# Performance work log

Hardware: AMD Instinct MI355X
Metric: run time of the kernel (lower is better)

## Reference

```python
import jax, jax.numpy as jnp
import numpy as np

B, S, H, KVH, D = 1, 2048, 32, 8, 128
ROPE_THETA = 500000.0


def _rotate_half(x):
    x1, x2 = jnp.split(x, 2, axis=-1)
    return jnp.concatenate((-x2, x1), axis=-1)


def setup_inputs() -> dict:
    key = jax.random.key(0)
    ks = jax.random.split(key, 5)
    hidden_states = jax.random.normal(ks[0], (B, S, H * D), dtype=jnp.float32)
    Wq = jax.random.normal(ks[1], (H * D, H * D), dtype=jnp.float32) * 0.02
    Wk = jax.random.normal(ks[2], (KVH * D, H * D), dtype=jnp.float32) * 0.02
    Wv = jax.random.normal(ks[3], (KVH * D, H * D), dtype=jnp.float32) * 0.02
    Wo = jax.random.normal(ks[4], (H * D, H * D), dtype=jnp.float32) * 0.02
    # rotary tables (Llama-style, concat of freqs with itself)
    inv_freq = 1.0 / (ROPE_THETA ** (jnp.arange(0, D, 2, dtype=jnp.float32) / D))
    freqs = jnp.arange(S, dtype=jnp.float32)[:, None] * inv_freq[None, :]  # [S, D/2]
    emb = jnp.concatenate((freqs, freqs), axis=-1)  # [S, D]
    cos = jnp.cos(emb)[None]  # [1, S, D]
    sin = jnp.sin(emb)[None]
    # additive causal mask, matching SDPA attn_mask semantics
    causal = jnp.tril(jnp.ones((S, S), dtype=bool))
    attention_mask = jnp.where(causal, 0.0, -1e9).astype(jnp.float32)[None, None]  # [1,1,S,S]
    return {"hidden_states": hidden_states, "attention_mask": attention_mask,
            "cos": cos, "sin": sin, "Wq": Wq, "Wk": Wk, "Wv": Wv, "Wo": Wo}


def reference(hidden_states, attention_mask, cos, sin, Wq, Wk, Wv, Wo):
    b, s, _ = hidden_states.shape
    d = cos.shape[-1]
    h = Wq.shape[0] // d
    kvh = Wk.shape[0] // d
    g = h // kvh  # GQA group size

    # fused QKV projection (nn.Linear: y = x @ W^T), then split heads -> [b, heads, s, d]
    q = jnp.einsum('bsi,oi->bso', hidden_states, Wq).reshape(b, s, h, d).transpose(0, 2, 1, 3)
    k = jnp.einsum('bsi,oi->bso', hidden_states, Wk).reshape(b, s, kvh, d).transpose(0, 2, 1, 3)
    v = jnp.einsum('bsi,oi->bso', hidden_states, Wv).reshape(b, s, kvh, d).transpose(0, 2, 1, 3)

    # rotary embedding (unsqueeze_dim=1)
    c = cos[:, None]  # [b,1,s,d]
    sn = sin[:, None]
    q = q * c + _rotate_half(q) * sn
    k = k * c + _rotate_half(k) * sn

    # GQA: view q as [b, kvh, g, s, d]; contract against un-repeated k/v
    qg = q.reshape(b, kvh, g, s, d)
    scale = 1.0 / jnp.sqrt(jnp.float32(d))
    scores = jnp.einsum('bkgsd,bktd->bkgst', qg, k) * scale  # [b,kvh,g,s,s]
    scores = scores + attention_mask[:, :, None]  # broadcast [b,1,1,s,s]
    probs = jax.nn.softmax(scores, axis=-1)
    attn = jnp.einsum('bkgst,bktd->bkgsd', probs, v)  # [b,kvh,g,s,d]

    attn = attn.reshape(b, h, s, d).transpose(0, 2, 1, 3).reshape(b, s, h * d)
    out = jnp.einsum('bso,po->bsp', attn, Wo)
    return out
```

## Files before the change

kernel.cpp:

```cpp
#include <hip/hip_runtime.h>
#include <hip/hip_bf16.h>

#define SEQ 2048
#define HD  128
#define NH  32
#define NKV 8
#define MODEL 4096
#define KVDIM 1024
#define QKVN 6144

typedef __attribute__((ext_vector_type(8))) short short8;
typedef __attribute__((ext_vector_type(4))) short short4v;
typedef __attribute__((ext_vector_type(4))) float float4v;

#define MFMA16(a, b, c) __builtin_amdgcn_mfma_f32_16x16x32_bf16(a, b, c, 0, 0, 0)

__device__ __forceinline__ short f2bf(float x) {
  unsigned u = __builtin_bit_cast(unsigned, x);
  u += 0x7fffu + ((u >> 16) & 1u);
  return (short)(u >> 16);
}
__device__ __forceinline__ float bf2f(short s) {
  unsigned u = ((unsigned)(unsigned short)s) << 16;
  return __builtin_bit_cast(float, u);
}

__device__ __forceinline__ void async_copy16(const void* g, void* l) {
  __builtin_amdgcn_global_load_lds((const __attribute__((address_space(1))) void*)g,
                                   (__attribute__((address_space(3))) void*)l, 16, 0, 0);
}

__global__ __launch_bounds__(256) void cast_bf16(const float* __restrict__ in,
                                                 short* __restrict__ out, int n) {
  int i = (blockIdx.x * 256 + threadIdx.x) * 4;
  if (i < n) {
    float4v v = *(const float4v*)(in + i);
    short4v o;
    o[0] = f2bf(v[0]); o[1] = f2bf(v[1]); o[2] = f2bf(v[2]); o[3] = f2bf(v[3]);
    *(short4v*)(out + i) = o;
  }
}

__global__ __launch_bounds__(512, 2) void gemm256(const short* __restrict__ A,
                                                  const short* __restrict__ B,
                                                  short* __restrict__ C,
                                                  int M, int N, int K) {
  __shared__ __align__(16) short As[2][256 * 64];
  __shared__ __align__(16) short Bs[2][256 * 64];
  const int tid = threadIdx.x;
  const int lane = tid & 63, w = tid >> 6;
  const int col = lane & 15, quad = lane >> 4;
  const int wm = w >> 2, wn = w & 3;

  const int nbx = N >> 8;
  int bid = blockIdx.x, nwg = gridDim.x;
  int swz = (nwg & 7) ? bid : ((bid & 7) * (nwg >> 3) + (bid >> 3));
  const int m0 = (swz / nbx) << 8;
  const int n0 = (swz % nbx) << 8;

  const int srow = tid >> 3;
  const int schunk = (tid & 7) ^ (srow & 7);
  const short* pA = A + (size_t)(m0 + srow) * K + schunk * 8;
  const short* pB = B + (size_t)(n0 + srow) * K + schunk * 8;
  const int ldst = tid * 8;

  const int sw = (col & 7) << 3;
  const int kof0 = (quad * 8) ^ sw;
  const int kof1 = (32 + quad * 8) ^ sw;
  const int ra = wm * 128, rb = wn * 64;

  float4v acc[8][4] = {};
  const int iters = K >> 6;

#define SA(buf, rA, kt) async_copy16(pA + (size_t)(rA) * K + (kt), &As[buf][(rA) * 64 + ldst])
#define SB_(buf, rB, kt) async_copy16(pB + (size_t)(rB) * K + (kt), &Bs[buf][(rB) * 64 + ldst])

  SA(0, 0, 0);  SA(0, 128, 0);
  SB_(0, 0, 0); SB_(0, 64, 0); SB_(0, 128, 0); SB_(0, 192, 0);
  SA(0, 64, 0); SA(0, 192, 0);
  asm volatile("s_waitcnt vmcnt(2)" ::: "memory");
  __builtin_amdgcn_s_barrier();

  for (int t = 0; t < iters; ++t) {
    const int cb = t & 1, nb = cb ^ 1;
    const int kt = (t + 1) << 6;
    const bool pf = (t + 1 < iters);
    const short* a_ = As[cb];
    const short* b_ = Bs[cb];
    short8 af[4][2], bf0[2][2], bf1[2][2];

#pragma unroll
    for (int mi = 0; mi < 4; ++mi) {
      const short* rp = a_ + (ra + mi * 16 + col) * 64;
      af[mi][0] = *(const short8*)(rp + kof0);
      af[mi][1] = *(const short8*)(rp + kof1);
    }
#pragma unroll
    for (int ni = 0; ni < 2; ++ni) {
      const short* rp = b_ + (rb + ni * 16 + col) * 64;
      bf0[ni][0] = *(const short8*)(rp + kof0);
      bf0[ni][1] = *(const short8*)(rp + kof1);
    }
    if (pf) { SA(nb, 0, kt); SA(nb, 128, kt); }
    __builtin_amdgcn_s_barrier();
    asm volatile("s_waitcnt lgkmcnt(0)" ::: "memory");
    __builtin_amdgcn_sched_barrier(0);
    __builtin_amdgcn_s_setprio(1);
#pragma unroll
    for (int mi = 0; mi < 4; ++mi)
#pragma unroll
      for (int ni = 0; ni < 2; ++ni) {
        acc[mi][ni] = MFMA16(af[mi][0], bf0[ni][0], acc[mi][ni]);
        acc[mi][ni] = MFMA16(af[mi][1], bf0[ni][1], acc[mi][ni]);
      }
    __builtin_amdgcn_s_setprio(0);
    __builtin_amdgcn_s_barrier();

#pragma unroll
    for (int ni = 0; ni < 2; ++ni) {
      const short* rp = b_ + (rb + (ni + 2) * 16 + col) * 64;
      bf1[ni][0] = *(const short8*)(rp + kof0);
      bf1[ni][1] = *(const short8*)(rp + kof1);
    }
    if (pf) { SB_(nb, 0, kt); SB_(nb, 64, kt); }
    __builtin_amdgcn_s_barrier();
    asm volatile("s_waitcnt lgkmcnt(0)" ::: "memory");
    __builtin_amdgcn_sched_barrier(0);
    __builtin_amdgcn_s_setprio(1);
#pragma unroll
    for (int mi = 0; mi < 4; ++mi)
#pragma unroll
      for (int ni = 0; ni < 2; ++ni) {
        acc[mi][ni + 2] = MFMA16(af[mi][0], bf1[ni][0], acc[mi][ni + 2]);
        acc[mi][ni + 2] = MFMA16(af[mi][1], bf1[ni][1], acc[mi][ni + 2]);
      }
    __builtin_amdgcn_s_setprio(0);
    if (pf) asm volatile("s_waitcnt vmcnt(4)" ::: "memory");
    else    asm volatile("s_waitcnt vmcnt(0)" ::: "memory");
    __builtin_amdgcn_s_barrier();

#pragma unroll
    for (int mi = 0; mi < 4; ++mi) {
      const short* rp = a_ + (ra + (mi + 4) * 16 + col) * 64;
      af[mi][0] = *(const short8*)(rp + kof0);
      af[mi][1] = *(const short8*)(rp + kof1);
    }
    if (pf) { SB_(nb, 128, kt); SB_(nb, 192, kt); }
    __builtin_amdgcn_s_barrier();
    asm volatile("s_waitcnt lgkmcnt(0)" ::: "memory");
    __builtin_amdgcn_sched_barrier(0);
    __builtin_amdgcn_s_setprio(1);
#pragma unroll
    for (int mi = 0; mi < 4; ++mi)
#pragma unroll
      for (int ni = 0; ni < 2; ++ni) {
        acc[mi + 4][ni + 2] = MFMA16(af[mi][0], bf1[ni][0], acc[mi + 4][ni + 2]);
        acc[mi + 4][ni + 2] = MFMA16(af[mi][1], bf1[ni][1], acc[mi + 4][ni + 2]);
      }
    __builtin_amdgcn_s_setprio(0);
    __builtin_amdgcn_s_barrier();

    if (pf) { SA(nb, 64, kt); SA(nb, 192, kt); }
    __builtin_amdgcn_s_setprio(1);
#pragma unroll
    for (int mi = 0; mi < 4; ++mi)
#pragma unroll
      for (int ni = 0; ni < 2; ++ni) {
        acc[mi + 4][ni] = MFMA16(af[mi][0], bf0[ni][0], acc[mi + 4][ni]);
        acc[mi + 4][ni] = MFMA16(af[mi][1], bf0[ni][1], acc[mi + 4][ni]);
      }
    __builtin_amdgcn_s_setprio(0);
    if (pf) asm volatile("s_waitcnt vmcnt(2)" ::: "memory");
    __builtin_amdgcn_s_barrier();
  }
#undef SA
#undef SB_

#pragma unroll
  for (int mi = 0; mi < 8; ++mi)
#pragma unroll
    for (int ni = 0; ni < 4; ++ni)
#pragma unroll
      for (int r = 0; r < 4; ++r) {
        int row = m0 + ra + mi * 16 + quad * 4 + r;
        int cc  = n0 + rb + ni * 16 + col;
        C[(size_t)row * N + cc] = f2bf(acc[mi][ni][r]);
      }
}

#define BM 128
#define BN 128
#define BK 32

__device__ __forceinline__ void store_out(float* C, size_t idx, float v) { C[idx] = v; }
__device__ __forceinline__ void store_out(short* C, size_t idx, float v) { C[idx] = f2bf(v); }

template <typename OUT>
__global__ __launch_bounds__(256) void gemm_nt(const short* __restrict__ A,
                                               const short* __restrict__ B,
                                               OUT* __restrict__ C,
                                               int M, int N, int K) {
  __shared__ __align__(16) short As[2][BM * BK];
  __shared__ __align__(16) short Bs[2][BN * BK];
  int t = threadIdx.x;
  int w = t >> 6, lane = t & 63;
  int col = lane & 15, quad = lane >> 4;
  int m0 = blockIdx.y * BM, n0 = blockIdx.x * BN;
  int wr = (w >> 1) * 64, wc = (w & 1) * 64;

  int srow   = lane >> 2;
  int schunk = (lane & 3) ^ ((lane >> 3) & 3);
  const short* Ag0 = A + (size_t)(m0 + w * 32 + srow) * K + schunk * 8;
  const short* Ag1 = Ag0 + (size_t)16 * K;
  const short* Bg0 = B + (size_t)(n0 + w * 32 + srow) * K + schunk * 8;
  const short* Bg1 = Bg0 + (size_t)16 * K;
  const int wofs0 = (w * 32) * BK;
  const int wofs1 = (w * 32 + 16) * BK;

  int aswz = (quad ^ ((col >> 1) & 3)) * 8;

  float4v acc[4][4] = {};

  async_copy16(Ag0, &As[0][wofs0]);
  async_copy16(Ag1, &As[0][wofs1]);
  async_copy16(Bg0, &Bs[0][wofs0]);
  async_copy16(Bg1, &Bs[0][wofs1]);
  __syncthreads();

  const int iters = K / BK;
  for (int it = 0; it < iters; it++) {
    const int cb = it & 1, nb = cb ^ 1;
    if (it + 1 < iters) {
      const int k0 = (it + 1) * BK;
      async_copy16(Ag0 + k0, &As[nb][wofs0]);
      async_copy16(Ag1 + k0, &As[nb][wofs1]);
      async_copy16(Bg0 + k0, &Bs[nb][wofs0]);
      async_copy16(Bg1 + k0, &Bs[nb][wofs1]);
    }
    short8 af[4], bfr[4];
#pragma unroll
    for (int i = 0; i < 4; i++)
      af[i] = *(const short8*)&As[cb][(wr + i * 16 + col) * BK + aswz];
#pragma unroll
    for (int i = 0; i < 4; i++)
      bfr[i] = *(const short8*)&Bs[cb][(wc + i * 16 + col) * BK + aswz];
#pragma unroll
    for (int mi = 0; mi < 4; mi++)
#pragma unroll
      for (int ni = 0; ni < 4; ni++)
        acc[mi][ni] = MFMA16(af[mi], bfr[ni], acc[mi][ni]);
    __syncthreads();
  }

#pragma unroll
  for (int mi = 0; mi < 4; mi++)
#pragma unroll
    for (int ni = 0; ni < 4; ni++)
#pragma unroll
      for (int r = 0; r < 4; r++) {
        int row = m0 + wr + mi * 16 + quad * 4 + r;
        int cc  = n0 + wc + ni * 16 + col;
        store_out(C, (size_t)row * N + cc, acc[mi][ni][r]);
      }
}

__global__ __launch_bounds__(128) void rope_kernel(const short* __restrict__ qkv,
                                                   const float* __restrict__ cosp,
                                                   const float* __restrict__ sinp,
                                                   short* __restrict__ qb,
                                                   short* __restrict__ kb) {
  int s = blockIdx.x, head = blockIdx.y, d = threadIdx.x;
  float c  = cosp[s * HD + d];
  float sn = sinp[s * HD + d];
  if (head < NH) {
    const short* base = qkv + (size_t)s * QKVN + head * HD;
    float x = bf2f(base[d]);
    float rot = (d < 64) ? -bf2f(base[d + 64]) : bf2f(base[d - 64]);
    qb[((size_t)(head * SEQ + s)) * HD + d] = f2bf((x * c + rot * sn) * 0.08838834764831845f);
  } else {
    int hk = head - NH;
    const short* base = qkv + (size_t)s * QKVN + MODEL + hk * HD;
    float x = bf2f(base[d]);
    float rot = (d < 64) ? -bf2f(base[d + 64]) : bf2f(base[d - 64]);
    kb[((size_t)(hk * SEQ + s)) * HD + d] = f2bf(x * c + rot * sn);
  }
}

__global__ __launch_bounds__(256) void vtrans_kernel(const short* __restrict__ qkv,
                                                     short* __restrict__ vt) {
  __shared__ short tile[32][34];
  int kv = blockIdx.z;
  int d0 = blockIdx.x * 32, s0 = blockIdx.y * 32;
  int tx = threadIdx.x, ty = threadIdx.y;
#pragma unroll
  for (int j = 0; j < 32; j += 8)
    tile[ty + j][tx] = qkv[(size_t)(s0 + ty + j) * QKVN + MODEL + KVDIM + kv * HD + d0 + tx];
  __syncthreads();
#pragma unroll
  for (int j = 0; j < 32; j += 8)
    vt[((size_t)(kv * HD + d0 + ty + j)) * SEQ + s0 + tx] = tile[tx][ty + j];
}

#define FKT 32
#define KLD 136
#define VLD 40
#define PLD 40

__global__ __launch_bounds__(256, 3) void flash_attn(const short* __restrict__ qb_,
                                                     const short* __restrict__ kb,
                                                     const short* __restrict__ vt,
                                                     short* __restrict__ attn) {
  __shared__ __align__(16) short Ks[2][FKT * KLD];
  __shared__ __align__(16) short Vs[2][HD * VLD];
  __shared__ __align__(16) short Ps[4][32 * PLD];
  const int tid = threadIdx.x;
  const int w = tid >> 6, lane = tid & 63;
  const int col = lane & 15, quad = lane >> 4;
  const int h = blockIdx.x;
  const int kv = h >> 2;
  const int yp = (blockIdx.y < 8) ? (15 - (int)blockIdx.y) : ((int)blockIdx.y - 8);
  const int qB0 = yp * 128;
  const int q0w = qB0 + w * 32;
  const int ntiles = qB0 / FKT + 4;

  short8 ones;
#pragma unroll
  for (int i = 0; i < 8; i++) ones[i] = (short)0x3F80;

  short8 qf[2][4];
  const short* qbase = qb_ + ((size_t)(h * SEQ + q0w + col)) * HD;
#pragma unroll
  for (int rt = 0; rt < 2; rt++)
#pragma unroll
    for (int ks = 0; ks < 4; ks++)
      qf[rt][ks] = *(const short8*)(qbase + rt * 16 * HD + ks * 32 + quad * 8);

  float4v o[2][8] = {};
  float4v la[2] = {};

  const int kg_off = tid * 8;
  const int klds0  = (kg_off >> 7) * KLD + (kg_off & 127);
  const int vd     = tid >> 2;
  const int vkof   = (tid & 3) * 8;
  const size_t vrow0 = ((size_t)(kv * HD + vd)) * SEQ;
  const size_t vrow1 = ((size_t)(kv * HD + vd + 64)) * SEQ;
  const int vlds0 = vd * VLD + vkof;
  const short* kgbase = kb + ((size_t)kv * SEQ) * HD;

  short8 kr0, kr1, vr0, vr1;
  kr0 = *(const short8*)(kgbase + kg_off);
  kr1 = *(const short8*)(kgbase + 2048 + kg_off);
  vr0 = *(const short8*)(vt + vrow0 + vkof);
  vr1 = *(const short8*)(vt + vrow1 + vkof);
  *(short8*)&Ks[0][klds0]            = kr0;
  *(short8*)&Ks[0][klds0 + 16 * KLD] = kr1;
  *(short8*)&Vs[0][vlds0]            = vr0;
  *(short8*)&Vs[0][vlds0 + 64 * VLD] = vr1;
  __syncthreads();

  for (int kt = 0; kt < ntiles; kt++) {
    const int b = kt & 1;
    const int key0 = kt * FKT;
    if (kt + 1 < ntiles) {
      const int nk0 = key0 + FKT;
      const short* kg = kgbase + (size_t)nk0 * HD;
      kr0 = *(const short8*)(kg + kg_off);
      kr1 = *(const short8*)(kg + 2048 + kg_off);
      vr0 = *(const short8*)(vt + vrow0 + nk0 + vkof);
      vr1 = *(const short8*)(vt + vrow1 + nk0 + vkof);
    }
    if (key0 <= q0w + 31) {
      float4v sct[2][2] = {};
#pragma unroll
      for (int ks = 0; ks < 4; ks++) {
        short8 kf0 = *(const short8*)&Ks[b][col * KLD + ks * 32 + quad * 8];
        short8 kf1 = *(const short8*)&Ks[b][(16 + col) * KLD + ks * 32 + quad * 8];
        sct[0][0] = MFMA16(kf0, qf[0][ks], sct[0][0]);
        sct[0][1] = MFMA16(kf0, qf[1][ks], sct[0][1]);
        sct[1][0] = MFMA16(kf1, qf[0][ks], sct[1][0]);
        sct[1][1] = MFMA16(kf1, qf[1][ks], sct[1][1]);
      }
      short* pw = Ps[w];
#pragma unroll
      for (int rt = 0; rt < 2; rt++) {
        int qrow = q0w + rt * 16 + col;
#pragma unroll
        for (int kt2 = 0; kt2 < 2; kt2++) {
          int keyb = key0 + kt2 * 16 + quad * 4;
          short4v p;
#pragma unroll
          for (int r = 0; r < 4; r++) {
            float s = sct[kt2][rt][r];
            if (keyb + r > qrow) s = -INFINITY;
            p[r] = f2bf(__expf(s));
          }
          *(short4v*)&pw[(rt * 16 + col) * PLD + kt2 * 16 + quad * 4] = p;
        }
      }
      asm volatile("s_waitcnt lgkmcnt(0)" ::: "memory");
      short8 pf0 = *(const short8*)&pw[col * PLD + quad * 8];
      short8 pf1 = *(const short8*)&pw[(16 + col) * PLD + quad * 8];
      la[0] = MFMA16(ones, pf0, la[0]);
      la[1] = MFMA16(ones, pf1, la[1]);
#pragma unroll
      for (int nc = 0; nc < 8; nc++) {
        short8 vb = *(const short8*)&Vs[b][(nc * 16 + col) * VLD + quad * 8];
        o[0][nc] = MFMA16(vb, pf0, o[0][nc]);
        o[1][nc] = MFMA16(vb, pf1, o[1][nc]);
      }
    }
    if (kt + 1 < ntiles) {
      const int nb = 1 - b;
      *(short8*)&Ks[nb][klds0]            = kr0;
      *(short8*)&Ks[nb][klds0 + 16 * KLD] = kr1;
      *(short8*)&Vs[nb][vlds0]            = vr0;
      *(short8*)&Vs[nb][vlds0 + 64 * VLD] = vr1;
    }
    __syncthreads();
  }

#pragma unroll
  for (int rt = 0; rt < 2; rt++) {
    float inv = 1.0f / la[rt][0];
    size_t rowbase = (size_t)(q0w + rt * 16 + col) * MODEL + h * HD + quad * 4;
#pragma unroll
    for (int nc = 0; nc < 8; nc++) {
      short4v ov;
#pragma unroll
      for (int r = 0; r < 4; r++) ov[r] = f2bf(o[rt][nc][r] * inv);
      *(short4v*)(attn + rowbase + nc * 16) = ov;
    }
  }
}

extern "C" void kernel_launch(void* const* d_in, const int* in_sizes, int n_in,
                              void* d_out, int out_size, void* d_ws, size_t ws_size,
                              hipStream_t stream) {
  const float* hidden = (const float*)d_in[0];
  const float* cosp = (const float*)d_in[2];
  const float* sinp = (const float*)d_in[3];
  const float* Wq   = (const float*)d_in[4];
  const float* Wk   = (const float*)d_in[5];
  const float* Wv   = (const float*)d_in[6];
  const float* Wo   = (const float*)d_in[7];

  char* ws = (char*)d_ws;
  size_t off = 0;
  auto alloc = [&](size_t bytes) {
    char* p = ws + off;
    off += (bytes + 255) & ~(size_t)255;
    return p;
  };
  short* wq_bf = (short*)alloc((size_t)MODEL * MODEL * 2);
  short* wk_bf = (short*)alloc((size_t)KVDIM * MODEL * 2);
  short* wv_bf = (short*)alloc((size_t)KVDIM * MODEL * 2);
  short* wo_bf = (short*)alloc((size_t)MODEL * MODEL * 2);
  short* h_bf  = (short*)alloc((size_t)SEQ * MODEL * 2);
  short* qkv_bf = (short*)alloc((size_t)SEQ * QKVN * 2);
  short* k_bf  = (short*)alloc((size_t)NKV * SEQ * HD * 2);
  short* v_t   = (short*)alloc((size_t)NKV * HD * SEQ * 2);
  short* attn_bf = (short*)alloc((size_t)SEQ * MODEL * 2);
  short* q_bf    = h_bf;

  {
    int n;
    n = SEQ * MODEL;    cast_bf16<<<n / 1024, 256, 0, stream>>>(hidden, h_bf, n);
    n = MODEL * MODEL;  cast_bf16<<<n / 1024, 256, 0, stream>>>(Wq, wq_bf, n);
    n = KVDIM * MODEL;  cast_bf16<<<n / 1024, 256, 0, stream>>>(Wk, wk_bf, n);
    n = KVDIM * MODEL;  cast_bf16<<<n / 1024, 256, 0, stream>>>(Wv, wv_bf, n);
    n = MODEL * MODEL;  cast_bf16<<<n / 1024, 256, 0, stream>>>(Wo, wo_bf, n);
  }

  gemm256<<<dim3((SEQ / 256) * (QKVN / 256)), 512, 0, stream>>>(h_bf, wq_bf, qkv_bf, SEQ, QKVN, MODEL);

  rope_kernel<<<dim3(SEQ, NH + NKV), 128, 0, stream>>>(qkv_bf, cosp, sinp, q_bf, k_bf);
  vtrans_kernel<<<dim3(HD / 32, SEQ / 32, NKV), dim3(32, 8), 0, stream>>>(qkv_bf, v_t);

  flash_attn<<<dim3(NH, SEQ / 128), 256, 0, stream>>>(q_bf, k_bf, v_t, attn_bf);

  gemm_nt<float><<<dim3(MODEL / BN, SEQ / BM), 256, 0, stream>>>(attn_bf, wo_bf, (float*)d_out, SEQ, MODEL, MODEL);
}
```

Before: 531.2 us.

## Template 256-row GEMM on N-tile width; use it for QKV and output projections

The 256x256 pipelined GEMM becomes a template on the number of 16-wide N fragments per wave. The QKV projection now uses 256x192 tiles, giving 256 workgroups instead of 192, which fills more compute units. The output projection drops the simpler 128x128 double-buffered GEMM and uses the 256x128 pipelined kernel with fp32 stores. The A-fragment loads are now split into four phases of two rows each, which adds barriers, and the smaller B tiles lower arithmetic intensity per workgroup.

```diff
diff --git a/kernel.cpp b/kernel.cpp
--- a/kernel.cpp
+++ b/kernel.cpp
@@ -41,22 +41,27 @@
   }
 }
 
-__global__ __launch_bounds__(512, 2) void gemm256(const short* __restrict__ A,
-                                                  const short* __restrict__ B,
-                                                  short* __restrict__ C,
-                                                  int M, int N, int K) {
+__device__ __forceinline__ void store_out(float* C, size_t idx, float v) { C[idx] = v; }
+__device__ __forceinline__ void store_out(short* C, size_t idx, float v) { C[idx] = f2bf(v); }
+
+template <int NI, typename OUT>
+__global__ __launch_bounds__(512, 2) void gemm256v(const short* __restrict__ A,
+                                                   const short* __restrict__ B,
+                                                   OUT* __restrict__ C,
+                                                   int M, int N, int K) {
+  constexpr int BN = NI * 64;
   __shared__ __align__(16) short As[2][256 * 64];
-  __shared__ __align__(16) short Bs[2][256 * 64];
+  __shared__ __align__(16) short Bs[2][BN * 64];
   const int tid = threadIdx.x;
   const int lane = tid & 63, w = tid >> 6;
   const int col = lane & 15, quad = lane >> 4;
   const int wm = w >> 2, wn = w & 3;
 
-  const int nbx = N >> 8;
+  const int nbx = N / BN;
   int bid = blockIdx.x, nwg = gridDim.x;
   int swz = (nwg & 7) ? bid : ((bid & 7) * (nwg >> 3) + (bid >> 3));
   const int m0 = (swz / nbx) << 8;
-  const int n0 = (swz % nbx) << 8;
+  const int n0 = (swz % nbx) * BN;
 
   const int srow = tid >> 3;
   const int schunk = (tid & 7) ^ (srow & 7);
@@ -67,16 +72,17 @@
   const int sw = (col & 7) << 3;
   const int kof0 = (quad * 8) ^ sw;
   const int kof1 = (32 + quad * 8) ^ sw;
-  const int ra = wm * 128, rb = wn * 64;
-
-  float4v acc[8][4] = {};
+  const int ra = wm * 128, rb = wn * (NI * 16);
+
+  float4v acc[8][NI] = {};
   const int iters = K >> 6;
 
 #define SA(buf, rA, kt) async_copy16(pA + (size_t)(rA) * K + (kt), &As[buf][(rA) * 64 + ldst])
 #define SB_(buf, rB, kt) async_copy16(pB + (size_t)(rB) * K + (kt), &Bs[buf][(rB) * 64 + ldst])
 
   SA(0, 0, 0);  SA(0, 128, 0);
-  SB_(0, 0, 0); SB_(0, 64, 0); SB_(0, 128, 0); SB_(0, 192, 0);
+  SB_(0, 0, 0); SB_(0, 64, 0);
+  if constexpr (NI == 3) SB_(0, 128, 0);
   SA(0, 64, 0); SA(0, 192, 0);
   asm volatile("s_waitcnt vmcnt(2)" ::: "memory");
   __builtin_amdgcn_s_barrier();
@@ -87,19 +93,20 @@
     const bool pf = (t + 1 < iters);
     const short* a_ = As[cb];
     const short* b_ = Bs[cb];
-    short8 af[4][2], bf0[2][2], bf1[2][2];
-
-#pragma unroll
-    for (int mi = 0; mi < 4; ++mi) {
-      const short* rp = a_ + (ra + mi * 16 + col) * 64;
-      af[mi][0] = *(const short8*)(rp + kof0);
-      af[mi][1] = *(const short8*)(rp + kof1);
-    }
-#pragma unroll
-    for (int ni = 0; ni < 2; ++ni) {
+    short8 bf[NI][2];
+    short8 af[2][2];
+
+#pragma unroll
+    for (int j = 0; j < 2; ++j) {
+      const short* rp = a_ + (ra + j * 16 + col) * 64;
+      af[j][0] = *(const short8*)(rp + kof0);
+      af[j][1] = *(const short8*)(rp + kof1);
+    }
+#pragma unroll
+    for (int ni = 0; ni < NI; ++ni) {
       const short* rp = b_ + (rb + ni * 16 + col) * 64;
-      bf0[ni][0] = *(const short8*)(rp + kof0);
-      bf0[ni][1] = *(const short8*)(rp + kof1);
+      bf[ni][0] = *(const short8*)(rp + kof0);
+      bf[ni][1] = *(const short8*)(rp + kof1);
     }
     if (pf) { SA(nb, 0, kt); SA(nb, 128, kt); }
     __builtin_amdgcn_s_barrier();
@@ -107,20 +114,20 @@
     __builtin_amdgcn_sched_barrier(0);
     __builtin_amdgcn_s_setprio(1);
 #pragma unroll
-    for (int mi = 0; mi < 4; ++mi)
-#pragma unroll
-      for (int ni = 0; ni < 2; ++ni) {
-        acc[mi][ni] = MFMA16(af[mi][0], bf0[ni][0], acc[mi][ni]);
-        acc[mi][ni] = MFMA16(af[mi][1], bf0[ni][1], acc[mi][ni]);
+    for (int j = 0; j < 2; ++j)
+#pragma unroll
+      for (int ni = 0; ni < NI; ++ni) {
+        acc[j][ni] = MFMA16(af[j][0], bf[ni][0], acc[j][ni]);
+        acc[j][ni] = MFMA16(af[j][1], bf[ni][1], acc[j][ni]);
       }
     __builtin_amdgcn_s_setprio(0);
     __builtin_amdgcn_s_barrier();
 
 #pragma unroll
-    for (int ni = 0; ni < 2; ++ni) {
-      const short* rp = b_ + (rb + (ni + 2) * 16 + col) * 64;
-      bf1[ni][0] = *(const short8*)(rp + kof0);
-      bf1[ni][1] = *(const short8*)(rp + kof1);
+    for (int j = 0; j < 2; ++j) {
+      const short* rp = a_ + (ra + (2 + j) * 16 + col) * 64;
+      af[j][0] = *(const short8*)(rp + kof0);
+      af[j][1] = *(const short8*)(rp + kof1);
     }
     if (pf) { SB_(nb, 0, kt); SB_(nb, 64, kt); }
     __builtin_amdgcn_s_barrier();
@@ -128,11 +135,11 @@
     __builtin_amdgcn_sched_barrier(0);
     __builtin_amdgcn_s_setprio(1);
 #pragma unroll
-    for (int mi = 0; mi < 4; ++mi)
-#pragma unroll
-      for (int ni = 0; ni < 2; ++ni) {
-        acc[mi][ni + 2] = MFMA16(af[mi][0], bf1[ni][0], acc[mi][ni + 2]);
-        acc[mi][ni + 2] = MFMA16(af[mi][1], bf1[ni][1], acc[mi][ni + 2]);
+    for (int j = 0; j < 2; ++j)
+#pragma unroll
+      for (int ni = 0; ni < NI; ++ni) {
+        acc[2 + j][ni] = MFMA16(af[j][0], bf[ni][0], acc[2 + j][ni]);
+        acc[2 + j][ni] = MFMA16(af[j][1], bf[ni][1], acc[2 + j][ni]);
       }
     __builtin_amdgcn_s_setprio(0);
     if (pf) asm volatile("s_waitcnt vmcnt(4)" ::: "memory");
@@ -140,34 +147,43 @@
     __builtin_amdgcn_s_barrier();
 
 #pragma unroll
-    for (int mi = 0; mi < 4; ++mi) {
-      const short* rp = a_ + (ra + (mi + 4) * 16 + col) * 64;
-      af[mi][0] = *(const short8*)(rp + kof0);
-      af[mi][1] = *(const short8*)(rp + kof1);
-    }
-    if (pf) { SB_(nb, 128, kt); SB_(nb, 192, kt); }
+    for (int j = 0; j < 2; ++j) {
+      const short* rp = a_ + (ra + (4 + j) * 16 + col) * 64;
+      af[j][0] = *(const short8*)(rp + kof0);
+      af[j][1] = *(const short8*)(rp + kof1);
+    }
+    if (pf) { if constexpr (NI == 3) SB_(nb, 128, kt); }
     __builtin_amdgcn_s_barrier();
     asm volatile("s_waitcnt lgkmcnt(0)" ::: "memory");
     __builtin_amdgcn_sched_barrier(0);
     __builtin_amdgcn_s_setprio(1);
 #pragma unroll
-    for (int mi = 0; mi < 4; ++mi)
-#pragma unroll
-      for (int ni = 0; ni < 2; ++ni) {
-        acc[mi + 4][ni + 2] = MFMA16(af[mi][0], bf1[ni][0], acc[mi + 4][ni + 2]);
-        acc[mi + 4][ni + 2] = MFMA16(af[mi][1], bf1[ni][1], acc[mi + 4][ni + 2]);
+    for (int j = 0; j < 2; ++j)
+#pragma unroll
+      for (int ni = 0; ni < NI; ++ni) {
+        acc[4 + j][ni] = MFMA16(af[j][0], bf[ni][0], acc[4 + j][ni]);
+        acc[4 + j][ni] = MFMA16(af[j][1], bf[ni][1], acc[4 + j][ni]);
       }
     __builtin_amdgcn_s_setprio(0);
     __builtin_amdgcn_s_barrier();
 
+#pragma unroll
+    for (int j = 0; j < 2; ++j) {
+      const short* rp = a_ + (ra + (6 + j) * 16 + col) * 64;
+      af[j][0] = *(const short8*)(rp + kof0);
+      af[j][1] = *(const short8*)(rp + kof1);
+    }
     if (pf) { SA(nb, 64, kt); SA(nb, 192, kt); }
+    __builtin_amdgcn_s_barrier();
+    asm volatile("s_waitcnt lgkmcnt(0)" ::: "memory");
+    __builtin_amdgcn_sched_barrier(0);
     __builtin_amdgcn_s_setprio(1);
 #pragma unroll
-    for (int mi = 0; mi < 4; ++mi)
-#pragma unroll
-      for (int ni = 0; ni < 2; ++ni) {
-        acc[mi + 4][ni] = MFMA16(af[mi][0], bf0[ni][0], acc[mi + 4][ni]);
-        acc[mi + 4][ni] = MFMA16(af[mi][1], bf0[ni][1], acc[mi + 4][ni]);
+    for (int j = 0; j < 2; ++j)
+#pragma unroll
+      for (int ni = 0; ni < NI; ++ni) {
+        acc[6 + j][ni] = MFMA16(af[j][0], bf[ni][0], acc[6 + j][ni]);
+        acc[6 + j][ni] = MFMA16(af[j][1], bf[ni][1], acc[6 + j][ni]);
       }
     __builtin_amdgcn_s_setprio(0);
     if (pf) asm volatile("s_waitcnt vmcnt(2)" ::: "memory");
@@ -179,87 +195,11 @@
 #pragma unroll
   for (int mi = 0; mi < 8; ++mi)
 #pragma unroll
-    for (int ni = 0; ni < 4; ++ni)
+    for (int ni = 0; ni < NI; ++ni)
 #pragma unroll
       for (int r = 0; r < 4; ++r) {
         int row = m0 + ra + mi * 16 + quad * 4 + r;
         int cc  = n0 + rb + ni * 16 + col;
-        C[(size_t)row * N + cc] = f2bf(acc[mi][ni][r]);
-      }
-}
-
-#define BM 128
-#define BN 128
-#define BK 32
-
-__device__ __forceinline__ void store_out(float* C, size_t idx, float v) { C[idx] = v; }
-__device__ __forceinline__ void store_out(short* C, size_t idx, float v) { C[idx] = f2bf(v); }
-
-template <typename OUT>
-__global__ __launch_bounds__(256) void gemm_nt(const short* __restrict__ A,
-                                               const short* __restrict__ B,
-                                               OUT* __restrict__ C,
-                                               int M, int N, int K) {
-  __shared__ __align__(16) short As[2][BM * BK];
-  __shared__ __align__(16) short Bs[2][BN * BK];
-  int t = threadIdx.x;
-  int w = t >> 6, lane = t & 63;
-  int col = lane & 15, quad = lane >> 4;
-  int m0 = blockIdx.y * BM, n0 = blockIdx.x * BN;
-  int wr = (w >> 1) * 64, wc = (w & 1) * 64;
-
-  int srow   = lane >> 2;
-  int schunk = (lane & 3) ^ ((lane >> 3) & 3);
-  const short* Ag0 = A + (size_t)(m0 + w * 32 + srow) * K + schunk * 8;
-  const short* Ag1 = Ag0 + (size_t)16 * K;
-  const short* Bg0 = B + (size_t)(n0 + w * 32 + srow) * K + schunk * 8;
-  const short* Bg1 = Bg0 + (size_t)16 * K;
-  const int wofs0 = (w * 32) * BK;
-  const int wofs1 = (w * 32 + 16) * BK;
-
-  int aswz = (quad ^ ((col >> 1) & 3)) * 8;
-
-  float4v acc[4][4] = {};
-
-  async_copy16(Ag0, &As[0][wofs0]);
-  async_copy16(Ag1, &As[0][wofs1]);
-  async_copy16(Bg0, &Bs[0][wofs0]);
-  async_copy16(Bg1, &Bs[0][wofs1]);
-  __syncthreads();
-
-  const int iters = K / BK;
-  for (int it = 0; it < iters; it++) {
-    const int cb = it & 1, nb = cb ^ 1;
-    if (it + 1 < iters) {
-      const int k0 = (it + 1) * BK;
-      async_copy16(Ag0 + k0, &As[nb][wofs0]);
-      async_copy16(Ag1 + k0, &As[nb][wofs1]);
-      async_copy16(Bg0 + k0, &Bs[nb][wofs0]);
-      async_copy16(Bg1 + k0, &Bs[nb][wofs1]);
-    }
-    short8 af[4], bfr[4];
-#pragma unroll
-    for (int i = 0; i < 4; i++)
-      af[i] = *(const short8*)&As[cb][(wr + i * 16 + col) * BK + aswz];
-#pragma unroll
-    for (int i = 0; i < 4; i++)
-      bfr[i] = *(const short8*)&Bs[cb][(wc + i * 16 + col) * BK + aswz];
-#pragma unroll
-    for (int mi = 0; mi < 4; mi++)
-#pragma unroll
-      for (int ni = 0; ni < 4; ni++)
-        acc[mi][ni] = MFMA16(af[mi], bfr[ni], acc[mi][ni]);
-    __syncthreads();
-  }
-
-#pragma unroll
-  for (int mi = 0; mi < 4; mi++)
-#pragma unroll
-    for (int ni = 0; ni < 4; ni++)
-#pragma unroll
-      for (int r = 0; r < 4; r++) {
-        int row = m0 + wr + mi * 16 + quad * 4 + r;
-        int cc  = n0 + wc + ni * 16 + col;
         store_out(C, (size_t)row * N + cc, acc[mi][ni][r]);
       }
 }
@@ -471,12 +411,14 @@
     n = MODEL * MODEL;  cast_bf16<<<n / 1024, 256, 0, stream>>>(Wo, wo_bf, n);
   }
 
-  gemm256<<<dim3((SEQ / 256) * (QKVN / 256)), 512, 0, stream>>>(h_bf, wq_bf, qkv_bf, SEQ, QKVN, MODEL);
+  gemm256v<3, short><<<dim3((SEQ / 256) * (QKVN / 192)), 512, 0, stream>>>(
+      h_bf, wq_bf, qkv_bf, SEQ, QKVN, MODEL);
 
   rope_kernel<<<dim3(SEQ, NH + NKV), 128, 0, stream>>>(qkv_bf, cosp, sinp, q_bf, k_bf);
   vtrans_kernel<<<dim3(HD / 32, SEQ / 32, NKV), dim3(32, 8), 0, stream>>>(qkv_bf, v_t);
 
   flash_attn<<<dim3(NH, SEQ / 128), 256, 0, stream>>>(q_bf, k_bf, v_t, attn_bf);
 
-  gemm_nt<float><<<dim3(MODEL / BN, SEQ / BM), 256, 0, stream>>>(attn_bf, wo_bf, (float*)d_out, SEQ, MODEL, MODEL);
-}
+  gemm256v<2, float><<<dim3((SEQ / 256) * (MODEL / 128)), 512, 0, stream>>>(
+      attn_bf, wo_bf, (float*)d_out, SEQ, MODEL, MODEL);
+}
```

Result: slower. 542.6 us (+2.1%).
